# Optimization experiments

Measured on AMD Instinct MI355X. Metric: run time of the kernel, lower is better.

## Reference

```python
import jax, jax.numpy as jnp
import numpy as np

# db4 reconstruction filters (pywt convention): rec_lo = reversed(dec_lo),
# rec_hi[k] = (-1)^k * dec_lo[k]
REC_LO = [0.23037781330885523, 0.7148465705525415, 0.6308807679295904,
          -0.02798376941698385, -0.18703481171888114, 0.030841381835986965,
          0.032883011666982945, -0.010597401784997278]
REC_HI = [-0.010597401784997278, -0.032883011666982945, 0.030841381835986965,
          0.18703481171888114, -0.02798376941698385, -0.6308807679295904,
          0.7148465705525415, -0.23037781330885523]
FILT_LEN = 8


def _idwt1d(cA, cD, axis):
    """Periodized single-level inverse DWT along `axis`. N -> 2N."""
    cA = jnp.moveaxis(cA, axis, -1)
    cD = jnp.moveaxis(cD, axis, -1)
    N = cA.shape[-1]
    up_a = jnp.zeros(cA.shape[:-1] + (2 * N,), cA.dtype).at[..., ::2].set(cA)
    up_d = jnp.zeros(cD.shape[:-1] + (2 * N,), cD.dtype).at[..., ::2].set(cD)
    # circular synthesis: y[m] = sum_k g[k]*up_a[m-k] + h[k]*up_d[m-k]
    y = sum(REC_LO[k] * jnp.roll(up_a, k, axis=-1) +
            REC_HI[k] * jnp.roll(up_d, k, axis=-1) for k in range(FILT_LEN))
    y = jnp.roll(y, -(FILT_LEN - 2), axis=-1)  # phase alignment (periodization)
    return jnp.moveaxis(y, -1, axis)


def setup_inputs() -> dict:
    key = jax.random.key(0)
    x = jax.random.normal(key, (64, 256, 256, 16), dtype=jnp.float32)
    return {"x": x}


def reference(x):
    # x: [B, H, W, 4*C] with channel groups = (cA, cH, cV, cD)
    c = x.shape[-1] // 4
    cA, cH, cV, cD = (x[..., :c], x[..., c:2 * c],
                      x[..., 2 * c:3 * c], x[..., 3 * c:])
    lo = _idwt1d(cA, cH, axis=1)   # [B, 2H, W, C]
    hi = _idwt1d(cV, cD, axis=1)   # [B, 2H, W, C]
    return _idwt1d(lo, hi, axis=2)  # [B, 2H, 2W, C]
```

## Files before the change

kernel.cpp:

```cpp
#include <hip/hip_runtime.h>


#define RJ 8
#define N 256

__device__ __forceinline__ void fma4(float4& d, float s, const float4 a) {
  d.x = fmaf(s, a.x, d.x);
  d.y = fmaf(s, a.y, d.y);
  d.z = fmaf(s, a.z, d.z);
  d.w = fmaf(s, a.w, d.w);
}

__global__ __launch_bounds__(512, 4) void idwt2_sep_kernel(
    const float* __restrict__ x, float* __restrict__ out) {
  constexpr float LO[8] = {
      0.23037781330885523f,  0.7148465705525415f,  0.6308807679295904f,
      -0.02798376941698385f, -0.18703481171888114f, 0.030841381835986965f,
      0.032883011666982945f, -0.010597401784997278f};
  constexpr float HIW[8] = {
      -0.010597401784997278f, -0.032883011666982945f, 0.030841381835986965f,
      0.18703481171888114f,  -0.02798376941698385f,  -0.6308807679295904f,
      0.7148465705525415f,   -0.23037781330885523f};
  const float Lw[2][4] = {{LO[6], LO[4], LO[2], LO[0]},
                          {LO[7], LO[5], LO[3], LO[1]}};
  const float Hw[2][4] = {{HIW[6], HIW[4], HIW[2], HIW[0]},
                          {HIW[7], HIW[5], HIW[3], HIW[1]}};

  __shared__ float4 I[2][2][2][N];

  const int t = threadIdx.x;
  const int tcol = t & (N - 1);
  const int thalf = t >> 8;
  const int rg = blockIdx.x & 31;
  const int b = blockIdx.x >> 5;
  const int r0 = rg * RJ;

  const float4* xb =
      reinterpret_cast<const float4*>(x) + (size_t)b * N * N * 4;
  float4* ob = reinterpret_cast<float4*>(out) + (size_t)b * (2 * N) * (2 * N);

  const float4* xcolp = xb + (size_t)tcol * 4 + thalf * 2;

  float4 wa[4], wb_[4];
#pragma unroll
  for (int i = 0; i < 4; ++i) {
    const int gr = (r0 + i) & (N - 1);
    wa[i] = xcolp[(size_t)gr * (N * 4)];
    wb_[i] = xcolp[(size_t)gr * (N * 4) + 1];
  }

  auto p1_compute = [&](int i, float4& v0, float4& v1) {
#pragma unroll
    for (int sy = 0; sy < 4; ++sy) {
      const float4 a = wa[(i + sy) & 3];
      const float4 bb = wb_[(i + sy) & 3];
      if (sy == 0) {
        v0 = make_float4(Lw[0][0] * a.x, Lw[0][0] * a.y, Lw[0][0] * a.z,
                         Lw[0][0] * a.w);
        v1 = make_float4(Lw[1][0] * a.x, Lw[1][0] * a.y, Lw[1][0] * a.z,
                         Lw[1][0] * a.w);
        fma4(v0, Hw[0][0], bb);
        fma4(v1, Hw[1][0], bb);
      } else {
        fma4(v0, Lw[0][sy], a);
        fma4(v0, Hw[0][sy], bb);
        fma4(v1, Lw[1][sy], a);
        fma4(v1, Hw[1][sy], bb);
      }
    }
  };

  {
    float4 v0, v1;
    p1_compute(0, v0, v1);
    I[0][0][thalf][tcol] = v0;
    I[0][1][thalf][tcol] = v1;
  }
  __syncthreads();

  const int jx = t >> 1;
  const int q = t & 1;

#pragma unroll
  for (int i = 0; i < RJ; ++i) {
    if (i < RJ - 1) {
      const int gr = (r0 + i + 4) & (N - 1);
      wa[i & 3] = xcolp[(size_t)gr * (N * 4)];
      wb_[i & 3] = xcolp[(size_t)gr * (N * 4) + 1];
    }

    float4 o0 = make_float4(0.f, 0.f, 0.f, 0.f);
    float4 o1 = make_float4(0.f, 0.f, 0.f, 0.f);
#pragma unroll
    for (int s = 0; s < 4; ++s) {
      const int xc = (jx + s) & (N - 1);
      const float lq = q ? Lw[1][s] : Lw[0][s];
      const float hq = q ? Hw[1][s] : Hw[0][s];
      fma4(o0, lq, I[i & 1][0][0][xc]);
      fma4(o0, hq, I[i & 1][0][1][xc]);
      fma4(o1, lq, I[i & 1][1][0][xc]);
      fma4(o1, hq, I[i & 1][1][1][xc]);
    }
    const int orow = 2 * (r0 + i);
    ob[(size_t)orow * (2 * N) + t] = o0;
    ob[(size_t)(orow + 1) * (2 * N) + t] = o1;

    if (i < RJ - 1) {
      float4 v0, v1;
      p1_compute(i + 1, v0, v1);
      I[(i + 1) & 1][0][thalf][tcol] = v0;
      I[(i + 1) & 1][1][thalf][tcol] = v1;
      __syncthreads();
    }
  }
}

extern "C" void kernel_launch(void* const* d_in, const int* in_sizes, int n_in,
                              void* d_out, int out_size, void* d_ws,
                              size_t ws_size, hipStream_t stream) {
  const float* x = reinterpret_cast<const float*>(d_in[0]);
  float* out = reinterpret_cast<float*>(d_out);
  const int grid = 64 * (N / RJ);
  idwt2_sep_kernel<<<grid, 512, 0, stream>>>(x, out);
}
```

Before: 120.5 us.

## Process two rows per step and compute both output columns per thread

```diff
diff --git a/kernel.cpp b/kernel.cpp
--- a/kernel.cpp
+++ b/kernel.cpp
@@ -1,8 +1,8 @@
 #include <hip/hip_runtime.h>
 
 
+#define N 256
 #define RJ 8
-#define N 256
 
 __device__ __forceinline__ void fma4(float4& d, float s, const float4 a) {
   d.x = fmaf(s, a.x, d.x);
@@ -11,7 +11,7 @@
   d.w = fmaf(s, a.w, d.w);
 }
 
-__global__ __launch_bounds__(512, 4) void idwt2_sep_kernel(
+__global__ __launch_bounds__(512, 4) void idwt2_sep3_kernel(
     const float* __restrict__ x, float* __restrict__ out) {
   constexpr float LO[8] = {
       0.23037781330885523f,  0.7148465705525415f,  0.6308807679295904f,
@@ -29,89 +29,106 @@
   __shared__ float4 I[2][2][2][N];
 
   const int t = threadIdx.x;
-  const int tcol = t & (N - 1);
-  const int thalf = t >> 8;
   const int rg = blockIdx.x & 31;
   const int b = blockIdx.x >> 5;
   const int r0 = rg * RJ;
 
-  const float4* xb =
-      reinterpret_cast<const float4*>(x) + (size_t)b * N * N * 4;
+  const float4* xb = reinterpret_cast<const float4*>(x) + (size_t)b * N * N * 4;
   float4* ob = reinterpret_cast<float4*>(out) + (size_t)b * (2 * N) * (2 * N);
 
+  const int tcol = t & (N - 1);
+  const int thalf = t >> 8;
   const float4* xcolp = xb + (size_t)tcol * 4 + thalf * 2;
 
-  float4 wa[4], wb_[4];
+  float4 wA[4], wB[4];
 #pragma unroll
-  for (int i = 0; i < 4; ++i) {
-    const int gr = (r0 + i) & (N - 1);
-    wa[i] = xcolp[(size_t)gr * (N * 4)];
-    wb_[i] = xcolp[(size_t)gr * (N * 4) + 1];
+  for (int m = 0; m < 4; ++m) {
+    const int gr = (r0 + m) & (N - 1);
+    wA[m] = xcolp[(size_t)gr * (N * 4)];
+    wB[m] = xcolp[(size_t)gr * (N * 4) + 1];
+  }
+  float4 nA0, nB0, nA1, nB1;
+  {
+    int gr = (r0 + 4) & (N - 1);
+    nA0 = xcolp[(size_t)gr * (N * 4)];
+    nB0 = xcolp[(size_t)gr * (N * 4) + 1];
+    gr = (r0 + 5) & (N - 1);
+    nA1 = xcolp[(size_t)gr * (N * 4)];
+    nB1 = xcolp[(size_t)gr * (N * 4) + 1];
   }
 
-  auto p1_compute = [&](int i, float4& v0, float4& v1) {
+  auto p1 = [&](int j, int jr) {
+    float4 v0 = make_float4(0.f, 0.f, 0.f, 0.f);
+    float4 v1 = make_float4(0.f, 0.f, 0.f, 0.f);
 #pragma unroll
     for (int sy = 0; sy < 4; ++sy) {
-      const float4 a = wa[(i + sy) & 3];
-      const float4 bb = wb_[(i + sy) & 3];
-      if (sy == 0) {
-        v0 = make_float4(Lw[0][0] * a.x, Lw[0][0] * a.y, Lw[0][0] * a.z,
-                         Lw[0][0] * a.w);
-        v1 = make_float4(Lw[1][0] * a.x, Lw[1][0] * a.y, Lw[1][0] * a.z,
-                         Lw[1][0] * a.w);
-        fma4(v0, Hw[0][0], bb);
-        fma4(v1, Hw[1][0], bb);
-      } else {
-        fma4(v0, Lw[0][sy], a);
-        fma4(v0, Hw[0][sy], bb);
-        fma4(v1, Lw[1][sy], a);
-        fma4(v1, Hw[1][sy], bb);
+      const float4 a = wA[(j + sy) & 3];
+      const float4 bb = wB[(j + sy) & 3];
+      fma4(v0, Lw[0][sy], a);
+      fma4(v0, Hw[0][sy], bb);
+      fma4(v1, Lw[1][sy], a);
+      fma4(v1, Hw[1][sy], bb);
+    }
+    I[jr][0][thalf][tcol] = v0;
+    I[jr][1][thalf][tcol] = v1;
+  };
+
+  const int jx = t & (N - 1);
+  const int jrsel = t >> 8;
+
+#pragma unroll
+  for (int k = 0; k < RJ / 2; ++k) {
+    p1(2 * k + 0, 0);
+    wA[(2 * k) & 3] = nA0;
+    wB[(2 * k) & 3] = nB0;
+    p1(2 * k + 1, 1);
+    if (k < RJ / 2 - 1) {
+      wA[(2 * k + 1) & 3] = nA1;
+      wB[(2 * k + 1) & 3] = nB1;
+    }
+    __syncthreads();
+
+    if (k < RJ / 2 - 1) {
+      int gr = (r0 + 2 * k + 6) & (N - 1);
+      nA0 = xcolp[(size_t)gr * (N * 4)];
+      nB0 = xcolp[(size_t)gr * (N * 4) + 1];
+      if (k < RJ / 2 - 2) {
+        gr = (r0 + 2 * k + 7) & (N - 1);
+        nA1 = xcolp[(size_t)gr * (N * 4)];
+        nB1 = xcolp[(size_t)gr * (N * 4) + 1];
       }
     }
-  };
 
-  {
-    float4 v0, v1;
-    p1_compute(0, v0, v1);
-    I[0][0][thalf][tcol] = v0;
-    I[0][1][thalf][tcol] = v1;
-  }
-  __syncthreads();
-
-  const int jx = t >> 1;
-  const int q = t & 1;
-
-#pragma unroll
-  for (int i = 0; i < RJ; ++i) {
-    if (i < RJ - 1) {
-      const int gr = (r0 + i + 4) & (N - 1);
-      wa[i & 3] = xcolp[(size_t)gr * (N * 4)];
-      wb_[i & 3] = xcolp[(size_t)gr * (N * 4) + 1];
-    }
-
-    float4 o0 = make_float4(0.f, 0.f, 0.f, 0.f);
-    float4 o1 = make_float4(0.f, 0.f, 0.f, 0.f);
+    float4 o00 = make_float4(0.f, 0.f, 0.f, 0.f);
+    float4 o01 = make_float4(0.f, 0.f, 0.f, 0.f);
+    float4 o10 = make_float4(0.f, 0.f, 0.f, 0.f);
+    float4 o11 = make_float4(0.f, 0.f, 0.f, 0.f);
 #pragma unroll
     for (int s = 0; s < 4; ++s) {
       const int xc = (jx + s) & (N - 1);
-      const float lq = q ? Lw[1][s] : Lw[0][s];
-      const float hq = q ? Hw[1][s] : Hw[0][s];
-      fma4(o0, lq, I[i & 1][0][0][xc]);
-      fma4(o0, hq, I[i & 1][0][1][xc]);
-      fma4(o1, lq, I[i & 1][1][0][xc]);
-      fma4(o1, hq, I[i & 1][1][1][xc]);
+      const float4 l0 = I[jrsel][0][0][xc];
+      const float4 h0 = I[jrsel][0][1][xc];
+      const float4 l1 = I[jrsel][1][0][xc];
+      const float4 h1 = I[jrsel][1][1][xc];
+      const float L0 = Lw[0][s], L1 = Lw[1][s];
+      const float H0 = Hw[0][s], H1 = Hw[1][s];
+      fma4(o00, L0, l0);
+      fma4(o00, H0, h0);
+      fma4(o01, L1, l0);
+      fma4(o01, H1, h0);
+      fma4(o10, L0, l1);
+      fma4(o10, H0, h1);
+      fma4(o11, L1, l1);
+      fma4(o11, H1, h1);
     }
-    const int orow = 2 * (r0 + i);
-    ob[(size_t)orow * (2 * N) + t] = o0;
-    ob[(size_t)(orow + 1) * (2 * N) + t] = o1;
+    const int jy = r0 + 2 * k + jrsel;
+    const size_t base = (size_t)(2 * jy) * (2 * N) + 2 * jx;
+    ob[base] = o00;
+    ob[base + 1] = o01;
+    ob[base + 2 * N] = o10;
+    ob[base + 2 * N + 1] = o11;
 
-    if (i < RJ - 1) {
-      float4 v0, v1;
-      p1_compute(i + 1, v0, v1);
-      I[(i + 1) & 1][0][thalf][tcol] = v0;
-      I[(i + 1) & 1][1][thalf][tcol] = v1;
-      __syncthreads();
-    }
+    if (k < RJ / 2 - 1) __syncthreads();
   }
 }
 
@@ -121,5 +138,5 @@
   const float* x = reinterpret_cast<const float*>(d_in[0]);
   float* out = reinterpret_cast<float*>(d_out);
   const int grid = 64 * (N / RJ);
-  idwt2_sep_kernel<<<grid, 512, 0, stream>>>(x, out);
+  idwt2_sep3_kernel<<<grid, 512, 0, stream>>>(x, out);
 }
```

Measured after the change: 128.5 us. 1.07x slower.

## Process two rows per sync, prefetch deeper, swizzle blocks, non-temporal stores

Applied to the files above, without the earlier changes.

```diff
diff --git a/kernel.cpp b/kernel.cpp
--- a/kernel.cpp
+++ b/kernel.cpp
@@ -1,8 +1,11 @@
 #include <hip/hip_runtime.h>
 
 
-#define RJ 8
 #define N 256
+#define RJ 16
+#define NC (RJ / 2)
+
+typedef float nfloat4 __attribute__((ext_vector_type(4)));
 
 __device__ __forceinline__ void fma4(float4& d, float s, const float4 a) {
   d.x = fmaf(s, a.x, d.x);
@@ -11,7 +14,16 @@
   d.w = fmaf(s, a.w, d.w);
 }
 
-__global__ __launch_bounds__(512, 4) void idwt2_sep_kernel(
+__device__ __forceinline__ void nt_store4(const float4 v, float4* p) {
+  nfloat4 nv;
+  nv.x = v.x;
+  nv.y = v.y;
+  nv.z = v.z;
+  nv.w = v.w;
+  __builtin_nontemporal_store(nv, reinterpret_cast<nfloat4*>(p));
+}
+
+__global__ __launch_bounds__(512, 4) void idwt2_sep4_kernel(
     const float* __restrict__ x, float* __restrict__ out) {
   constexpr float LO[8] = {
       0.23037781330885523f,  0.7148465705525415f,  0.6308807679295904f,
@@ -26,90 +38,102 @@
   const float Hw[2][4] = {{HIW[6], HIW[4], HIW[2], HIW[0]},
                           {HIW[7], HIW[5], HIW[3], HIW[1]}};
 
-  __shared__ float4 I[2][2][2][N];
+  __shared__ float4 I[2][2][2][2][N];
 
   const int t = threadIdx.x;
+  const int bx = blockIdx.x;
+  const int orig = ((bx & 7) << 7) | (bx >> 3);
+  const int b = orig >> 4;
+  const int r0 = (orig & 15) * RJ;
+
+  const float4* xb = reinterpret_cast<const float4*>(x) + (size_t)b * N * N * 4;
+  float4* ob = reinterpret_cast<float4*>(out) + (size_t)b * (2 * N) * (2 * N);
+
   const int tcol = t & (N - 1);
   const int thalf = t >> 8;
-  const int rg = blockIdx.x & 31;
-  const int b = blockIdx.x >> 5;
-  const int r0 = rg * RJ;
-
-  const float4* xb =
-      reinterpret_cast<const float4*>(x) + (size_t)b * N * N * 4;
-  float4* ob = reinterpret_cast<float4*>(out) + (size_t)b * (2 * N) * (2 * N);
-
   const float4* xcolp = xb + (size_t)tcol * 4 + thalf * 2;
 
-  float4 wa[4], wb_[4];
+  float4 wA[4], wB[4], nA0, nB0, nA1, nB1;
+  auto ldrow = [&](int lr, float4& A, float4& B) {
+    const int gr = (r0 + lr) & (N - 1);
+    A = xcolp[(size_t)gr * (N * 4)];
+    B = xcolp[(size_t)gr * (N * 4) + 1];
+  };
+
 #pragma unroll
-  for (int i = 0; i < 4; ++i) {
-    const int gr = (r0 + i) & (N - 1);
-    wa[i] = xcolp[(size_t)gr * (N * 4)];
-    wb_[i] = xcolp[(size_t)gr * (N * 4) + 1];
-  }
+  for (int m = 0; m < 4; ++m) ldrow(m, wA[m], wB[m]);
+  ldrow(4, nA0, nB0);
+  ldrow(5, nA1, nB1);
 
-  auto p1_compute = [&](int i, float4& v0, float4& v1) {
+  auto p1 = [&](int j, int buf, int r) {
+    float4 v0 = make_float4(0.f, 0.f, 0.f, 0.f);
+    float4 v1 = make_float4(0.f, 0.f, 0.f, 0.f);
 #pragma unroll
     for (int sy = 0; sy < 4; ++sy) {
-      const float4 a = wa[(i + sy) & 3];
-      const float4 bb = wb_[(i + sy) & 3];
-      if (sy == 0) {
-        v0 = make_float4(Lw[0][0] * a.x, Lw[0][0] * a.y, Lw[0][0] * a.z,
-                         Lw[0][0] * a.w);
-        v1 = make_float4(Lw[1][0] * a.x, Lw[1][0] * a.y, Lw[1][0] * a.z,
-                         Lw[1][0] * a.w);
-        fma4(v0, Hw[0][0], bb);
-        fma4(v1, Hw[1][0], bb);
-      } else {
-        fma4(v0, Lw[0][sy], a);
-        fma4(v0, Hw[0][sy], bb);
-        fma4(v1, Lw[1][sy], a);
-        fma4(v1, Hw[1][sy], bb);
-      }
+      const float4 a = wA[(j + sy) & 3];
+      const float4 bb = wB[(j + sy) & 3];
+      fma4(v0, Lw[0][sy], a);
+      fma4(v0, Hw[0][sy], bb);
+      fma4(v1, Lw[1][sy], a);
+      fma4(v1, Hw[1][sy], bb);
     }
+    I[buf][r][0][thalf][tcol] = v0;
+    I[buf][r][1][thalf][tcol] = v1;
   };
 
-  {
-    float4 v0, v1;
-    p1_compute(0, v0, v1);
-    I[0][0][thalf][tcol] = v0;
-    I[0][1][thalf][tcol] = v1;
-  }
+  p1(0, 0, 0);
+  wA[0] = nA0;
+  wB[0] = nB0;
+  p1(1, 0, 1);
+  wA[1] = nA1;
+  wB[1] = nB1;
+  ldrow(6, nA0, nB0);
+  ldrow(7, nA1, nB1);
   __syncthreads();
 
   const int jx = t >> 1;
   const int q = t & 1;
+  float Lq[4], Hq[4];
+#pragma unroll
+  for (int s = 0; s < 4; ++s) {
+    Lq[s] = q ? Lw[1][s] : Lw[0][s];
+    Hq[s] = q ? Hw[1][s] : Hw[0][s];
+  }
+
+#pragma unroll 2
+  for (int c = 0; c < NC; ++c) {
+    const int buf = c & 1;
 
 #pragma unroll
-  for (int i = 0; i < RJ; ++i) {
-    if (i < RJ - 1) {
-      const int gr = (r0 + i + 4) & (N - 1);
-      wa[i & 3] = xcolp[(size_t)gr * (N * 4)];
-      wb_[i & 3] = xcolp[(size_t)gr * (N * 4) + 1];
+    for (int r = 0; r < 2; ++r) {
+      float4 o0 = make_float4(0.f, 0.f, 0.f, 0.f);
+      float4 o1 = make_float4(0.f, 0.f, 0.f, 0.f);
+#pragma unroll
+      for (int s = 0; s < 4; ++s) {
+        const int xc = (jx + s) & (N - 1);
+        fma4(o0, Lq[s], I[buf][r][0][0][xc]);
+        fma4(o0, Hq[s], I[buf][r][0][1][xc]);
+        fma4(o1, Lq[s], I[buf][r][1][0][xc]);
+        fma4(o1, Hq[s], I[buf][r][1][1][xc]);
+      }
+      const int jy = r0 + 2 * c + r;
+      float4* po = ob + (size_t)(2 * jy) * (2 * N) + t;
+      nt_store4(o0, po);
+      nt_store4(o1, po + 2 * N);
     }
 
-    float4 o0 = make_float4(0.f, 0.f, 0.f, 0.f);
-    float4 o1 = make_float4(0.f, 0.f, 0.f, 0.f);
-#pragma unroll
-    for (int s = 0; s < 4; ++s) {
-      const int xc = (jx + s) & (N - 1);
-      const float lq = q ? Lw[1][s] : Lw[0][s];
-      const float hq = q ? Hw[1][s] : Hw[0][s];
-      fma4(o0, lq, I[i & 1][0][0][xc]);
-      fma4(o0, hq, I[i & 1][0][1][xc]);
-      fma4(o1, lq, I[i & 1][1][0][xc]);
-      fma4(o1, hq, I[i & 1][1][1][xc]);
-    }
-    const int orow = 2 * (r0 + i);
-    ob[(size_t)orow * (2 * N) + t] = o0;
-    ob[(size_t)(orow + 1) * (2 * N) + t] = o1;
+    if (c < NC - 1) {
+      p1(2 * c + 2, buf ^ 1, 0);
+      wA[(2 * c + 2) & 3] = nA0;
+      wB[(2 * c + 2) & 3] = nB0;
+      p1(2 * c + 3, buf ^ 1, 1);
+      wA[(2 * c + 3) & 3] = nA1;
+      wB[(2 * c + 3) & 3] = nB1;
 
-    if (i < RJ - 1) {
-      float4 v0, v1;
-      p1_compute(i + 1, v0, v1);
-      I[(i + 1) & 1][0][thalf][tcol] = v0;
-      I[(i + 1) & 1][1][thalf][tcol] = v1;
+      if (c < NC - 2) {
+        ldrow(2 * c + 8, nA0, nB0);
+        if (2 * c + 9 <= RJ + 2) ldrow(2 * c + 9, nA1, nB1);
+      }
       __syncthreads();
     }
   }
@@ -121,5 +145,5 @@
   const float* x = reinterpret_cast<const float*>(d_in[0]);
   float* out = reinterpret_cast<float*>(d_out);
   const int grid = 64 * (N / RJ);
-  idwt2_sep_kernel<<<grid, 512, 0, stream>>>(x, out);
+  idwt2_sep4_kernel<<<grid, 512, 0, stream>>>(x, out);
 }
```

Measured after the change: 305.2 us. +153.2%, slower.
